# Optimization experiments

Hardware: AMD Instinct MI355X
Metric: run time of the kernel (lower is better)

Reference implementation:

```python
import jax, jax.numpy as jnp
import numpy as np

B, N, L, D = 4, 128, 20, 512


def setup_inputs() -> dict:
    key = jax.random.key(0)
    ks = jax.random.split(key, 8)
    return {
        "f_b": jax.random.normal(ks[0], (B, N, D), jnp.float32),
        "f_w": jax.random.normal(ks[1], (B, L, D), jnp.float32),
        "f_s": jax.random.normal(ks[2], (B, D), jnp.float32),
        "f_m": jax.random.normal(ks[3], (B, N, N, D), jnp.float32),
        "Wq": jax.random.normal(ks[4], (D, D), jnp.float32) / np.sqrt(D).astype(np.float32),
        "bq": jax.random.normal(ks[5], (D,), jnp.float32) * 0.02,
        "Wk": jax.random.normal(ks[6], (D, D), jnp.float32) / np.sqrt(D).astype(np.float32),
        "bk": jax.random.normal(ks[7], (D,), jnp.float32) * 0.02,
    }


def reference(f_b, f_w, f_s, f_m, Wq, bq, Wk, bk):
    d = f_b.shape[-1]
    scale = jnp.asarray(1.0 / np.sqrt(d), f_b.dtype)
    # cross-attention: boundary features attend to word features
    q = f_b @ Wq.T + bq                                   # [B,N,D]
    k = f_w @ Wk.T + bk                                   # [B,L,D]
    attn = jax.nn.softmax(jnp.einsum('bnd,bld->bnl', q, k) * scale, axis=-1)
    f_baq = jnp.einsum('bnl,bld->bnd', attn, f_w)         # [B,N,D]
    # sentence-gated boundary features
    f_bq = f_b * (f_baq + f_s[:, None, :])                # [B,N,D]
    # boundary self-attention
    A_b = jax.nn.softmax(jnp.einsum('bnd,bmd->bnm', f_bq, f_bq) * scale, axis=-1)
    f_bb = jnp.einsum('bnm,bmd->bnd', A_b, f_b)           # [B,N,D]
    # gated moment-map reduction: sum_i A_b[b,i,j] * sigmoid(f_m*f_s)*f_m
    g_m = jax.nn.sigmoid(f_m * f_s[:, None, None, :])     # [B,N,N,D]
    f_bm = jnp.einsum('bij,bijd->bjd', A_b, g_m * f_m)    # [B,N,D]
    return f_bb + f_b + f_bm
```

## Files before the change

### kernel.cpp

```cpp
#include <hip/hip_runtime.h>
#include <hip/hip_bf16.h>

#define Bc 4
#define Nc 128
#define Lc 20
#define Dc 512
#define SCALE 0.04419417382415922f
#define NL2E -1.4426950408889634f

#if __has_builtin(__builtin_amdgcn_exp2f)
#define EXP2(x) __builtin_amdgcn_exp2f(x)
#else
#define EXP2(x) __expf((x) * 0.6931471805599453f)
#endif

__global__ __launch_bounds__(256)
void proj_gemm(const float* __restrict__ f_b, const float* __restrict__ f_w,
               const float* __restrict__ Wq, const float* __restrict__ bq,
               const float* __restrict__ Wk, const float* __restrict__ bk,
               float* __restrict__ qb, float* __restrict__ kb) {
    const int t  = threadIdx.x;
    const int tr = blockIdx.y, tc = blockIdx.x;
    const int c0 = tc * 32;
    const bool isq = tr < 16;
    const float* Ain  = isq ? f_b : f_w;
    const float* W    = isq ? Wq : Wk;
    const float* bias = isq ? bq : bk;
    float* C          = isq ? qb : kb;
    const int r0    = isq ? tr * 32 : (tr - 16) * 32;
    const int nrows = isq ? 512 : 80;

    __shared__ __align__(16) float As[16 * 34];
    __shared__ __align__(16) float Bs[16 * 34];

    const int sr  = t >> 3;
    const int sk2 = (t & 7) * 2;
    const int arow = min(r0 + sr, nrows - 1);
    const int wrow = c0 + sr;

    const int ty2 = (t >> 4) * 2;
    const int tx2 = (t & 15) * 2;
    float a00 = 0.f, a01 = 0.f, a10 = 0.f, a11 = 0.f;

    for (int k0 = 0; k0 < Dc; k0 += 16) {
        const float2 ga = *(const float2*)&Ain[arow * Dc + k0 + sk2];
        const float2 gb = *(const float2*)&W[wrow * Dc + k0 + sk2];
        __syncthreads();
        As[sk2 * 34 + sr]       = ga.x;
        As[(sk2 + 1) * 34 + sr] = ga.y;
        Bs[sk2 * 34 + sr]       = gb.x;
        Bs[(sk2 + 1) * 34 + sr] = gb.y;
        __syncthreads();
#pragma unroll
        for (int kk = 0; kk < 16; kk++) {
            const float2 av = *(const float2*)&As[kk * 34 + ty2];
            const float2 bv = *(const float2*)&Bs[kk * 34 + tx2];
            a00 = fmaf(av.x, bv.x, a00); a01 = fmaf(av.x, bv.y, a01);
            a10 = fmaf(av.y, bv.x, a10); a11 = fmaf(av.y, bv.y, a11);
        }
    }
    const int orow = r0 + ty2;
    const float b0 = bias[c0 + tx2], b1 = bias[c0 + tx2 + 1];
    if (orow < nrows)
        *(float2*)&C[orow * Dc + c0 + tx2] = make_float2(a00 + b0, a01 + b1);
    if (orow + 1 < nrows)
        *(float2*)&C[(orow + 1) * Dc + c0 + tx2] = make_float2(a10 + b0, a11 + b1);
}

__global__ __launch_bounds__(256)
void cross_attn_gate(const float* __restrict__ q, const float* __restrict__ k,
                     const float* __restrict__ f_w, const float* __restrict__ f_b,
                     const float* __restrict__ f_s, float* __restrict__ f_bq) {
    const int bn = blockIdx.x;
    const int b  = bn >> 7;
    const int t  = threadIdx.x;
    const int lane = t & 63, wave = t >> 6;

    __shared__ __align__(16) float qs[Dc];
    __shared__ float sc[32];
    __shared__ float invs;

    ((float2*)qs)[t] = ((const float2*)(q + bn * Dc))[t];
    __syncthreads();

    const float4* q4 = (const float4*)qs;
    const float4 qa = q4[lane];
    const float4 qv = q4[lane + 64];

    for (int l = wave; l < Lc; l += 4) {
        const float4* kr = (const float4*)(k + (b * Lc + l) * Dc);
        const float4 ka = kr[lane];
        const float4 kv = kr[lane + 64];
        float s = qa.x * ka.x + qa.y * ka.y + qa.z * ka.z + qa.w * ka.w
                + qv.x * kv.x + qv.y * kv.y + qv.z * kv.z + qv.w * kv.w;
#pragma unroll
        for (int d = 32; d >= 1; d >>= 1) s += __shfl_down(s, d, 64);
        if (lane == 0) sc[l] = s * SCALE;
    }
    __syncthreads();

    if (t == 0) {
        float mx = sc[0];
        for (int l = 1; l < Lc; l++) mx = fmaxf(mx, sc[l]);
        float sum = 0.f;
        for (int l = 0; l < Lc; l++) { float e = __expf(sc[l] - mx); sc[l] = e; sum += e; }
        invs = 1.0f / sum;
    }
    __syncthreads();
    const float inv = invs;

    const float2* fw2 = (const float2*)(f_w + b * Lc * Dc);
    float2 acc = make_float2(0.f, 0.f);
#pragma unroll 5
    for (int l = 0; l < Lc; l++) {
        const float2 v = fw2[l * 256 + t];
        const float w = sc[l];
        acc.x = fmaf(w, v.x, acc.x);
        acc.y = fmaf(w, v.y, acc.y);
    }
    const float2 s2 = ((const float2*)(f_s + b * Dc))[t];
    const float2 fb2 = ((const float2*)(f_b + bn * Dc))[t];
    float2 o;
    o.x = fb2.x * (acc.x * inv + s2.x);
    o.y = fb2.y * (acc.y * inv + s2.y);
    ((float2*)(f_bq + bn * Dc))[t] = o;
}

__global__ __launch_bounds__(512)
void self_attn_scores(const float* __restrict__ f_bq,
                      float* __restrict__ A_b, float* __restrict__ A_bT) {
    const int bn = blockIdx.x;
    const int b  = bn >> 7, n = bn & 127;
    const int t  = threadIdx.x;
    const int lane = t & 63, wave = t >> 6;

    __shared__ __align__(16) float qrow[Dc];
    __shared__ float sc[Nc];
    __shared__ float red[Nc];

    qrow[t] = f_bq[bn * Dc + t];
    __syncthreads();

    const float4* q4 = (const float4*)qrow;
    const float4 qa = q4[lane];
    const float4 qv = q4[lane + 64];

    for (int m = wave; m < Nc; m += 8) {
        const float4* kr = (const float4*)(f_bq + (b * Nc + m) * Dc);
        const float4 va = kr[lane];
        const float4 vb = kr[lane + 64];
        float s = qa.x * va.x + qa.y * va.y + qa.z * va.z + qa.w * va.w
                + qv.x * vb.x + qv.y * vb.y + qv.z * vb.z + qv.w * vb.w;
#pragma unroll
        for (int d = 32; d >= 1; d >>= 1) s += __shfl_down(s, d, 64);
        if (lane == 0) sc[m] = s * SCALE;
    }
    __syncthreads();

    float e = 0.f, sval = 0.f;
    if (t < Nc) { sval = sc[t]; red[t] = sval; }
    __syncthreads();
    for (int st = 64; st >= 1; st >>= 1) {
        if (t < st) red[t] = fmaxf(red[t], red[t + st]);
        __syncthreads();
    }
    const float mx = red[0];
    __syncthreads();
    if (t < Nc) { e = __expf(sval - mx); red[t] = e; }
    __syncthreads();
    for (int st = 64; st >= 1; st >>= 1) {
        if (t < st) red[t] += red[t + st];
        __syncthreads();
    }
    if (t < Nc) {
        const float a = e * (1.0f / red[0]);
        A_b[bn * Nc + t] = a;
        A_bT[(b * Nc + t) * Nc + n] = a;
    }
}

__global__ __launch_bounds__(256)
void moment_final(const float* __restrict__ f_m, const float* __restrict__ f_s,
                  const float* __restrict__ A_b, const float* __restrict__ A_bT,
                  const float* __restrict__ f_b, float* __restrict__ out) {
    const int bj = blockIdx.x;
    const int b  = bj >> 7, j = bj & 127;
    const int dh = blockIdx.y;
    const int t  = threadIdx.x;
    const int c   = t & 63;
    const int qtr = t >> 6;

    __shared__ float w[Nc];
    __shared__ float ar[Nc];
    __shared__ __align__(16) float4 pex[3][64];

    if (t < Nc) w[t] = A_bT[bj * Nc + t];
    else if (t < 2 * Nc) ar[t - Nc] = A_b[bj * Nc + (t - Nc)];
    __syncthreads();

    const int c4 = dh * 64 + c;
    const float4 s4 = ((const float4*)(f_s + b * Dc))[c4];
    const float4 ns = make_float4(NL2E * s4.x, NL2E * s4.y, NL2E * s4.z, NL2E * s4.w);

    float4 acc = make_float4(0.f, 0.f, 0.f, 0.f);
    const float4* fm4 = (const float4*)f_m;
    int idx = ((b * Nc + qtr * 32) * Nc + j) * (Dc / 4) + c4;

#pragma unroll 8
    for (int i = 0; i < 32; i++) {
        const float4 m4 = fm4[idx];
        idx += Nc * (Dc / 4);
        const float ww = w[qtr * 32 + i];
        acc.x = fmaf(ww * m4.x, __builtin_amdgcn_rcpf(1.f + EXP2(m4.x * ns.x)), acc.x);
        acc.y = fmaf(ww * m4.y, __builtin_amdgcn_rcpf(1.f + EXP2(m4.y * ns.y)), acc.y);
        acc.z = fmaf(ww * m4.z, __builtin_amdgcn_rcpf(1.f + EXP2(m4.z * ns.z)), acc.z);
        acc.w = fmaf(ww * m4.w, __builtin_amdgcn_rcpf(1.f + EXP2(m4.w * ns.w)), acc.w);
    }

    const float4* fb4 = (const float4*)(f_b + b * Nc * Dc);
#pragma unroll 8
    for (int m = qtr * 32; m < qtr * 32 + 32; m++) {
        const float a = ar[m];
        const float4 v = fb4[m * (Dc / 4) + c4];
        acc.x = fmaf(a, v.x, acc.x); acc.y = fmaf(a, v.y, acc.y);
        acc.z = fmaf(a, v.z, acc.z); acc.w = fmaf(a, v.w, acc.w);
    }

    if (qtr != 0) pex[qtr - 1][c] = acc;
    __syncthreads();
    if (qtr == 0) {
        const float4 p0 = pex[0][c], p1 = pex[1][c], p2 = pex[2][c];
        const float4 r  = fb4[j * (Dc / 4) + c4];
        acc.x += p0.x + p1.x + p2.x + r.x;
        acc.y += p0.y + p1.y + p2.y + r.y;
        acc.z += p0.z + p1.z + p2.z + r.z;
        acc.w += p0.w + p1.w + p2.w + r.w;
        ((float4*)out)[bj * (Dc / 4) + c4] = acc;
    }
}

extern "C" void kernel_launch(void* const* d_in, const int* in_sizes, int n_in,
                              void* d_out, int out_size, void* d_ws, size_t ws_size,
                              hipStream_t stream) {
    const float* f_b = (const float*)d_in[0];
    const float* f_w = (const float*)d_in[1];
    const float* f_s = (const float*)d_in[2];
    const float* f_m = (const float*)d_in[3];
    const float* Wq  = (const float*)d_in[4];
    const float* bq  = (const float*)d_in[5];
    const float* Wk  = (const float*)d_in[6];
    const float* bk  = (const float*)d_in[7];
    float* out = (float*)d_out;

    float* ws   = (float*)d_ws;
    float* qb   = ws;
    float* kb   = qb   + 512 * Dc;
    float* f_bq = kb   + 80 * Dc;
    float* A_b  = f_bq + 512 * Dc;
    float* A_bT = A_b  + 512 * Nc;

    proj_gemm<<<dim3(16, 19), 256, 0, stream>>>(f_b, f_w, Wq, bq, Wk, bk, qb, kb);
    cross_attn_gate<<<Bc * Nc, 256, 0, stream>>>(qb, kb, f_w, f_b, f_s, f_bq);
    self_attn_scores<<<Bc * Nc, 512, 0, stream>>>(f_bq, A_b, A_bT);
    moment_final<<<dim3(Bc * Nc, 2), 256, 0, stream>>>(f_m, f_s, A_b, A_bT, f_b, out);
}
```

Baseline: 259.8 us.

## Split projection GEMM over K into two partial sums and prefetch global loads

```diff
diff --git a/kernel.cpp b/kernel.cpp
--- a/kernel.cpp
+++ b/kernel.cpp
@@ -18,17 +18,19 @@
 void proj_gemm(const float* __restrict__ f_b, const float* __restrict__ f_w,
                const float* __restrict__ Wq, const float* __restrict__ bq,
                const float* __restrict__ Wk, const float* __restrict__ bk,
-               float* __restrict__ qb, float* __restrict__ kb) {
-    const int t  = threadIdx.x;
-    const int tr = blockIdx.y, tc = blockIdx.x;
+               float* __restrict__ q1, float* __restrict__ q2,
+               float* __restrict__ k1, float* __restrict__ k2) {
+    const int t  = threadIdx.x;
+    const int tr = blockIdx.y, tc = blockIdx.x, kh = blockIdx.z;
     const int c0 = tc * 32;
     const bool isq = tr < 16;
     const float* Ain  = isq ? f_b : f_w;
     const float* W    = isq ? Wq : Wk;
     const float* bias = isq ? bq : bk;
-    float* C          = isq ? qb : kb;
+    float* C          = isq ? (kh ? q2 : q1) : (kh ? k2 : k1);
     const int r0    = isq ? tr * 32 : (tr - 16) * 32;
     const int nrows = isq ? 512 : 80;
+    const int kbase = kh * 256;
 
     __shared__ __align__(16) float As[16 * 34];
     __shared__ __align__(16) float Bs[16 * 34];
@@ -42,15 +44,22 @@
     const int tx2 = (t & 15) * 2;
     float a00 = 0.f, a01 = 0.f, a10 = 0.f, a11 = 0.f;
 
-    for (int k0 = 0; k0 < Dc; k0 += 16) {
-        const float2 ga = *(const float2*)&Ain[arow * Dc + k0 + sk2];
-        const float2 gb = *(const float2*)&W[wrow * Dc + k0 + sk2];
+    const float* Aptr = Ain + arow * Dc + kbase + sk2;
+    const float* Wptr = W   + wrow * Dc + kbase + sk2;
+    float2 ga = *(const float2*)Aptr;
+    float2 gb = *(const float2*)Wptr;
+
+    for (int kk0 = 16; kk0 <= 256; kk0 += 16) {
         __syncthreads();
         As[sk2 * 34 + sr]       = ga.x;
         As[(sk2 + 1) * 34 + sr] = ga.y;
         Bs[sk2 * 34 + sr]       = gb.x;
         Bs[(sk2 + 1) * 34 + sr] = gb.y;
         __syncthreads();
+        if (kk0 < 256) {
+            ga = *(const float2*)(Aptr + kk0);
+            gb = *(const float2*)(Wptr + kk0);
+        }
 #pragma unroll
         for (int kk = 0; kk < 16; kk++) {
             const float2 av = *(const float2*)&As[kk * 34 + ty2];
@@ -60,7 +69,8 @@
         }
     }
     const int orow = r0 + ty2;
-    const float b0 = bias[c0 + tx2], b1 = bias[c0 + tx2 + 1];
+    const float b0 = kh ? 0.f : bias[c0 + tx2];
+    const float b1 = kh ? 0.f : bias[c0 + tx2 + 1];
     if (orow < nrows)
         *(float2*)&C[orow * Dc + c0 + tx2] = make_float2(a00 + b0, a01 + b1);
     if (orow + 1 < nrows)
@@ -68,7 +78,8 @@
 }
 
 __global__ __launch_bounds__(256)
-void cross_attn_gate(const float* __restrict__ q, const float* __restrict__ k,
+void cross_attn_gate(const float* __restrict__ q1, const float* __restrict__ q2,
+                     const float* __restrict__ k1, const float* __restrict__ k2,
                      const float* __restrict__ f_w, const float* __restrict__ f_b,
                      const float* __restrict__ f_s, float* __restrict__ f_bq) {
     const int bn = blockIdx.x;
@@ -80,7 +91,11 @@
     __shared__ float sc[32];
     __shared__ float invs;
 
-    ((float2*)qs)[t] = ((const float2*)(q + bn * Dc))[t];
+    {
+        const float2 u = ((const float2*)(q1 + bn * Dc))[t];
+        const float2 v = ((const float2*)(q2 + bn * Dc))[t];
+        ((float2*)qs)[t] = make_float2(u.x + v.x, u.y + v.y);
+    }
     __syncthreads();
 
     const float4* q4 = (const float4*)qs;
@@ -88,9 +103,12 @@
     const float4 qv = q4[lane + 64];
 
     for (int l = wave; l < Lc; l += 4) {
-        const float4* kr = (const float4*)(k + (b * Lc + l) * Dc);
-        const float4 ka = kr[lane];
-        const float4 kv = kr[lane + 64];
+        const float4* kr1 = (const float4*)(k1 + (b * Lc + l) * Dc);
+        const float4* kr2 = (const float4*)(k2 + (b * Lc + l) * Dc);
+        const float4 ka1 = kr1[lane],      ka2 = kr2[lane];
+        const float4 kv1 = kr1[lane + 64], kv2 = kr2[lane + 64];
+        const float4 ka = make_float4(ka1.x + ka2.x, ka1.y + ka2.y, ka1.z + ka2.z, ka1.w + ka2.w);
+        const float4 kv = make_float4(kv1.x + kv2.x, kv1.y + kv2.y, kv1.z + kv2.z, kv1.w + kv2.w);
         float s = qa.x * ka.x + qa.y * ka.y + qa.z * ka.z + qa.w * ka.w
                 + qv.x * kv.x + qv.y * kv.y + qv.z * kv.z + qv.w * kv.w;
 #pragma unroll
@@ -253,14 +271,16 @@
     float* out = (float*)d_out;
 
     float* ws   = (float*)d_ws;
-    float* qb   = ws;
-    float* kb   = qb   + 512 * Dc;
-    float* f_bq = kb   + 80 * Dc;
+    float* q1   = ws;
+    float* q2   = q1   + 512 * Dc;
+    float* k1   = q2   + 512 * Dc;
+    float* k2   = k1   + 80 * Dc;
+    float* f_bq = k2   + 80 * Dc;
     float* A_b  = f_bq + 512 * Dc;
     float* A_bT = A_b  + 512 * Nc;
 
-    proj_gemm<<<dim3(16, 19), 256, 0, stream>>>(f_b, f_w, Wq, bq, Wk, bk, qb, kb);
-    cross_attn_gate<<<Bc * Nc, 256, 0, stream>>>(qb, kb, f_w, f_b, f_s, f_bq);
+    proj_gemm<<<dim3(16, 19, 2), 256, 0, stream>>>(f_b, f_w, Wq, bq, Wk, bk, q1, q2, k1, k2);
+    cross_attn_gate<<<Bc * Nc, 256, 0, stream>>>(q1, q2, k1, k2, f_w, f_b, f_s, f_bq);
     self_attn_scores<<<Bc * Nc, 512, 0, stream>>>(f_bq, A_b, A_bT);
     moment_final<<<dim3(Bc * Nc, 2), 256, 0, stream>>>(f_m, f_s, A_b, A_bT, f_b, out);
 }
```

After: 247.0 us. 1.05x faster.

## Split-K projection GEMM, register-prefetch loads, and finer moment_final grid

Applied to the files above, without the earlier changes.

```diff
diff --git a/kernel.cpp b/kernel.cpp
--- a/kernel.cpp
+++ b/kernel.cpp
@@ -20,15 +20,16 @@
                const float* __restrict__ Wk, const float* __restrict__ bk,
                float* __restrict__ qb, float* __restrict__ kb) {
     const int t  = threadIdx.x;
-    const int tr = blockIdx.y, tc = blockIdx.x;
+    const int tr = blockIdx.y, tc = blockIdx.x, kh = blockIdx.z;
     const int c0 = tc * 32;
     const bool isq = tr < 16;
     const float* Ain  = isq ? f_b : f_w;
     const float* W    = isq ? Wq : Wk;
     const float* bias = isq ? bq : bk;
-    float* C          = isq ? qb : kb;
+    float* C          = isq ? (qb + kh * 512 * Dc) : (kb + kh * 80 * Dc);
     const int r0    = isq ? tr * 32 : (tr - 16) * 32;
     const int nrows = isq ? 512 : 80;
+    const int kbase = kh * 128;
 
     __shared__ __align__(16) float As[16 * 34];
     __shared__ __align__(16) float Bs[16 * 34];
@@ -42,15 +43,22 @@
     const int tx2 = (t & 15) * 2;
     float a00 = 0.f, a01 = 0.f, a10 = 0.f, a11 = 0.f;
 
-    for (int k0 = 0; k0 < Dc; k0 += 16) {
-        const float2 ga = *(const float2*)&Ain[arow * Dc + k0 + sk2];
-        const float2 gb = *(const float2*)&W[wrow * Dc + k0 + sk2];
+    const float* Aptr = Ain + arow * Dc + kbase + sk2;
+    const float* Wptr = W   + wrow * Dc + kbase + sk2;
+    float2 ga = *(const float2*)Aptr;
+    float2 gb = *(const float2*)Wptr;
+
+    for (int kk0 = 16; kk0 <= 128; kk0 += 16) {
         __syncthreads();
         As[sk2 * 34 + sr]       = ga.x;
         As[(sk2 + 1) * 34 + sr] = ga.y;
         Bs[sk2 * 34 + sr]       = gb.x;
         Bs[(sk2 + 1) * 34 + sr] = gb.y;
         __syncthreads();
+        if (kk0 < 128) {
+            ga = *(const float2*)(Aptr + kk0);
+            gb = *(const float2*)(Wptr + kk0);
+        }
 #pragma unroll
         for (int kk = 0; kk < 16; kk++) {
             const float2 av = *(const float2*)&As[kk * 34 + ty2];
@@ -60,7 +68,8 @@
         }
     }
     const int orow = r0 + ty2;
-    const float b0 = bias[c0 + tx2], b1 = bias[c0 + tx2 + 1];
+    const float b0 = kh ? 0.f : bias[c0 + tx2];
+    const float b1 = kh ? 0.f : bias[c0 + tx2 + 1];
     if (orow < nrows)
         *(float2*)&C[orow * Dc + c0 + tx2] = make_float2(a00 + b0, a01 + b1);
     if (orow + 1 < nrows)
@@ -68,7 +77,7 @@
 }
 
 __global__ __launch_bounds__(256)
-void cross_attn_gate(const float* __restrict__ q, const float* __restrict__ k,
+void cross_attn_gate(const float* __restrict__ qb, const float* __restrict__ kb,
                      const float* __restrict__ f_w, const float* __restrict__ f_b,
                      const float* __restrict__ f_s, float* __restrict__ f_bq) {
     const int bn = blockIdx.x;
@@ -80,7 +89,15 @@
     __shared__ float sc[32];
     __shared__ float invs;
 
-    ((float2*)qs)[t] = ((const float2*)(q + bn * Dc))[t];
+    {
+        float2 s = make_float2(0.f, 0.f);
+#pragma unroll
+        for (int h = 0; h < 4; h++) {
+            const float2 u = ((const float2*)(qb + h * 512 * Dc + bn * Dc))[t];
+            s.x += u.x; s.y += u.y;
+        }
+        ((float2*)qs)[t] = s;
+    }
     __syncthreads();
 
     const float4* q4 = (const float4*)qs;
@@ -88,9 +105,16 @@
     const float4 qv = q4[lane + 64];
 
     for (int l = wave; l < Lc; l += 4) {
-        const float4* kr = (const float4*)(k + (b * Lc + l) * Dc);
-        const float4 ka = kr[lane];
-        const float4 kv = kr[lane + 64];
+        float4 ka = make_float4(0.f, 0.f, 0.f, 0.f);
+        float4 kv = make_float4(0.f, 0.f, 0.f, 0.f);
+#pragma unroll
+        for (int h = 0; h < 4; h++) {
+            const float4* kr = (const float4*)(kb + h * 80 * Dc + (b * Lc + l) * Dc);
+            const float4 u = kr[lane];
+            const float4 v = kr[lane + 64];
+            ka.x += u.x; ka.y += u.y; ka.z += u.z; ka.w += u.w;
+            kv.x += v.x; kv.y += v.y; kv.z += v.z; kv.w += v.w;
+        }
         float s = qa.x * ka.x + qa.y * ka.y + qa.z * ka.z + qa.w * ka.w
                 + qv.x * kv.x + qv.y * kv.y + qv.z * kv.z + qv.w * kv.w;
 #pragma unroll
@@ -179,38 +203,38 @@
     }
 }
 
-__global__ __launch_bounds__(256)
+__global__ __launch_bounds__(256, 8)
 void moment_final(const float* __restrict__ f_m, const float* __restrict__ f_s,
                   const float* __restrict__ A_b, const float* __restrict__ A_bT,
                   const float* __restrict__ f_b, float* __restrict__ out) {
     const int bj = blockIdx.x;
     const int b  = bj >> 7, j = bj & 127;
-    const int dh = blockIdx.y;
-    const int t  = threadIdx.x;
-    const int c   = t & 63;
-    const int qtr = t >> 6;
+    const int dq = blockIdx.y;
+    const int t  = threadIdx.x;
+    const int c  = t & 31;
+    const int g  = t >> 5;
 
     __shared__ float w[Nc];
     __shared__ float ar[Nc];
-    __shared__ __align__(16) float4 pex[3][64];
+    __shared__ __align__(16) float4 pex[7][32];
 
     if (t < Nc) w[t] = A_bT[bj * Nc + t];
-    else if (t < 2 * Nc) ar[t - Nc] = A_b[bj * Nc + (t - Nc)];
-    __syncthreads();
-
-    const int c4 = dh * 64 + c;
+    else        ar[t - Nc] = A_b[bj * Nc + (t - Nc)];
+    __syncthreads();
+
+    const int c4 = dq * 32 + c;
     const float4 s4 = ((const float4*)(f_s + b * Dc))[c4];
     const float4 ns = make_float4(NL2E * s4.x, NL2E * s4.y, NL2E * s4.z, NL2E * s4.w);
 
     float4 acc = make_float4(0.f, 0.f, 0.f, 0.f);
     const float4* fm4 = (const float4*)f_m;
-    int idx = ((b * Nc + qtr * 32) * Nc + j) * (Dc / 4) + c4;
-
-#pragma unroll 8
-    for (int i = 0; i < 32; i++) {
+    int idx = ((b * Nc + g * 16) * Nc + j) * (Dc / 4) + c4;
+
+#pragma unroll 4
+    for (int i = 0; i < 16; i++) {
         const float4 m4 = fm4[idx];
         idx += Nc * (Dc / 4);
-        const float ww = w[qtr * 32 + i];
+        const float ww = w[g * 16 + i];
         acc.x = fmaf(ww * m4.x, __builtin_amdgcn_rcpf(1.f + EXP2(m4.x * ns.x)), acc.x);
         acc.y = fmaf(ww * m4.y, __builtin_amdgcn_rcpf(1.f + EXP2(m4.y * ns.y)), acc.y);
         acc.z = fmaf(ww * m4.z, __builtin_amdgcn_rcpf(1.f + EXP2(m4.z * ns.z)), acc.z);
@@ -218,23 +242,24 @@
     }
 
     const float4* fb4 = (const float4*)(f_b + b * Nc * Dc);
-#pragma unroll 8
-    for (int m = qtr * 32; m < qtr * 32 + 32; m++) {
+#pragma unroll 4
+    for (int m = g * 16; m < g * 16 + 16; m++) {
         const float a = ar[m];
         const float4 v = fb4[m * (Dc / 4) + c4];
         acc.x = fmaf(a, v.x, acc.x); acc.y = fmaf(a, v.y, acc.y);
         acc.z = fmaf(a, v.z, acc.z); acc.w = fmaf(a, v.w, acc.w);
     }
 
-    if (qtr != 0) pex[qtr - 1][c] = acc;
-    __syncthreads();
-    if (qtr == 0) {
-        const float4 p0 = pex[0][c], p1 = pex[1][c], p2 = pex[2][c];
-        const float4 r  = fb4[j * (Dc / 4) + c4];
-        acc.x += p0.x + p1.x + p2.x + r.x;
-        acc.y += p0.y + p1.y + p2.y + r.y;
-        acc.z += p0.z + p1.z + p2.z + r.z;
-        acc.w += p0.w + p1.w + p2.w + r.w;
+    if (g != 0) pex[g - 1][c] = acc;
+    __syncthreads();
+    if (g == 0) {
+#pragma unroll
+        for (int p = 0; p < 7; p++) {
+            const float4 q = pex[p][c];
+            acc.x += q.x; acc.y += q.y; acc.z += q.z; acc.w += q.w;
+        }
+        const float4 r = fb4[j * (Dc / 4) + c4];
+        acc.x += r.x; acc.y += r.y; acc.z += r.z; acc.w += r.w;
         ((float4*)out)[bj * (Dc / 4) + c4] = acc;
     }
 }
@@ -254,13 +279,13 @@
 
     float* ws   = (float*)d_ws;
     float* qb   = ws;
-    float* kb   = qb   + 512 * Dc;
-    float* f_bq = kb   + 80 * Dc;
+    float* kb   = qb   + 4 * 512 * Dc;
+    float* f_bq = kb   + 4 * 80 * Dc;
     float* A_b  = f_bq + 512 * Dc;
     float* A_bT = A_b  + 512 * Nc;
 
-    proj_gemm<<<dim3(16, 19), 256, 0, stream>>>(f_b, f_w, Wq, bq, Wk, bk, qb, kb);
+    proj_gemm<<<dim3(16, 19, 4), 256, 0, stream>>>(f_b, f_w, Wq, bq, Wk, bk, qb, kb);
     cross_attn_gate<<<Bc * Nc, 256, 0, stream>>>(qb, kb, f_w, f_b, f_s, f_bq);
     self_attn_scores<<<Bc * Nc, 512, 0, stream>>>(f_bq, A_b, A_bT);
-    moment_final<<<dim3(Bc * Nc, 2), 256, 0, stream>>>(f_m, f_s, A_b, A_bT, f_b, out);
-}
+    moment_final<<<dim3(Bc * Nc, 4), 256, 0, stream>>>(f_m, f_s, A_b, A_bT, f_b, out);
+}
```

Result: faster. 243.1 us, median of 2 (-6.4%).
